# Kernel tuning notes

Hardware: AMD Instinct MI355X
Metric: run time of the kernel (lower is better)

## Reference

```python
import jax, jax.numpy as jnp
import numpy as np

B, T, D, S, K_FUT = 32, 1024, 1024, 256, 3


def setup_inputs() -> dict:
    key = jax.random.key(0)
    ks = jax.random.split(key, 8)
    sc = 1.0 / np.sqrt(D)
    return {
        "features": jax.random.normal(ks[0], (B, T, D), jnp.float32),
        "codebook": jax.random.uniform(ks[1], (S, D), jnp.float32, -1.0 / S, 1.0 / S),
        "W_ih": jax.random.normal(ks[2], (3 * D, D), jnp.float32) * sc,
        "W_hh": jax.random.normal(ks[3], (3 * D, D), jnp.float32) * sc,
        "b_ih": jnp.zeros((3 * D,), jnp.float32),
        "b_hh": jnp.zeros((3 * D,), jnp.float32),
        "W_p": jax.random.normal(ks[4], (D, D), jnp.float32) * sc,
        "b_p": jnp.zeros((D,), jnp.float32),
        "neg_idx": jax.random.randint(ks[5], (K_FUT, T, B), 0, B, jnp.int32),
    }


def _gru(x, W_ih, W_hh, b_ih, b_hh):
    # x: (B, T, D) -> outputs (B, T, D), torch nn.GRU gate math
    d = x.shape[-1]
    xs = jnp.swapaxes(x, 0, 1)  # (T, B, D)
    h0 = jnp.zeros((x.shape[0], d), x.dtype)

    def step(h, xt):
        gi = xt @ W_ih.T + b_ih
        gh = h @ W_hh.T + b_hh
        i_r, i_z, i_n = jnp.split(gi, 3, axis=-1)
        h_r, h_z, h_n = jnp.split(gh, 3, axis=-1)
        r = jax.nn.sigmoid(i_r + h_r)
        z = jax.nn.sigmoid(i_z + h_z)
        n = jnp.tanh(i_n + r * h_n)
        h_new = (1.0 - z) * n + z * h
        return h_new, h_new

    _, hs = jax.lax.scan(step, h0, xs)
    return jnp.swapaxes(hs, 0, 1)  # (B, T, D)


def _quantize(features, codebook):
    # argmin of euclidean distance == argmin of squared distance
    flat = features.reshape(-1, features.shape[-1])  # (B*T, D)
    d2 = (
        jnp.sum(flat * flat, -1, keepdims=True)
        - 2.0 * flat @ codebook.T
        + jnp.sum(codebook * codebook, -1)[None, :]
    )  # (B*T, S)
    idx = jnp.argmin(d2, axis=-1)
    quantized = codebook[idx].reshape(features.shape)
    return quantized, idx.reshape(features.shape[:2])


def _cp_loss(features, quantized, neg_idx, W_ih, W_hh, b_ih, b_hh, W_p, b_p):
    Bb, Tt, _ = features.shape
    H = _gru(quantized, W_ih, W_hh, b_ih, b_hh)
    Hp = H @ W_p.T + b_p  # (B, T, D)
    Zt = jnp.swapaxes(features, 0, 1)  # (T, B, D)
    K = min(K_FUT, Tt - 1)
    total = jnp.float32(0.0)
    for k in range(1, K + 1):
        pos = jnp.sum(Hp[:, : Tt - k] * features[:, k:], axis=-1)  # (B, T-k)
        idx = neg_idx[k - 1, : Tt - k]  # (T-k, B)
        negZ = jnp.take_along_axis(Zt[: Tt - k], idx[:, :, None], axis=1)  # (T-k, B, D)
        neg = jnp.sum(Hp[:, : Tt - k] * jnp.swapaxes(negZ, 0, 1), axis=-1)  # (B, T-k)
        per_tau = -jnp.log(jax.nn.sigmoid(pos - neg).mean(axis=0))  # (T-k,)
        total = total + per_tau.sum()
    return total / (K * (Tt - K))


def reference(features, codebook, W_ih, W_hh, b_ih, b_hh, W_p, b_p, neg_idx):
    quantized, indices = _quantize(features, codebook)
    cp = _cp_loss(features, quantized, neg_idx, W_ih, W_hh, b_ih, b_hh, W_p, b_p)
    sg = jax.lax.stop_gradient
    commitment = jnp.mean((sg(features) - quantized) ** 2)
    codebook_l = jnp.mean((features - sg(quantized)) ** 2)
    total = cp + commitment + 0.25 * codebook_l
    return quantized, indices, total
```

## Files before the change

kernel.cpp:

```cpp
#include <hip/hip_runtime.h>
#include <stdint.h>

#define DIM   1024
#define TLEN  1024
#define BATCH 32
#define NCODE 256

#define WS_CC   16
#define WS_IDX  272
#define WS_CGI  33040
#define WS_H    819472
#define WS_HP   34373904

#define OUT_IDX 33554432
#define OUT_TOT 33587200

__global__ __launch_bounds__(256) void k_norms(const float* __restrict__ cb,
                                               float* __restrict__ cc) {
  int c = blockIdx.x;
  int t = threadIdx.x;
  const float4* p = (const float4*)(cb + (size_t)c * DIM);
  float4 v = p[t];
  float s = v.x*v.x + v.y*v.y + v.z*v.z + v.w*v.w;
#pragma unroll
  for (int m = 1; m < 64; m <<= 1) s += __shfl_xor(s, m);
  __shared__ float ls[4];
  if ((t & 63) == 0) ls[t >> 6] = s;
  __syncthreads();
  if (t == 0) cc[c] = ls[0] + ls[1] + ls[2] + ls[3];
}

__global__ __launch_bounds__(256) void k_quant(
    const float* __restrict__ F, const float* __restrict__ CB,
    const float* __restrict__ cc, float* __restrict__ qout,
    float* __restrict__ idxf, int* __restrict__ idxi,
    float* __restrict__ sse_acc)
{
  __shared__ float Fl[32][33];
  __shared__ float Cl[256][33];
  __shared__ float ccl[256];
  __shared__ float sumff[32];
  __shared__ unsigned long long rowmin[32];
  __shared__ float wsum[4];

  const int tid = threadIdx.x;
  const size_t m0 = (size_t)blockIdx.x * 32;

  const int tm = tid >> 5;
  const int tn = tid & 31;
  const int ar = tid >> 3;
  const int ac = tid & 7;

  if (tid < 32) rowmin[tid] = ~0ull;
  ccl[tid] = cc[tid];

  float acc[4][8];
#pragma unroll
  for (int i = 0; i < 4; ++i)
#pragma unroll
    for (int j = 0; j < 8; ++j) acc[i][j] = 0.f;
  float ffp = 0.f;

  for (int k0 = 0; k0 < DIM; k0 += 32) {
    __syncthreads();
    {
      float4 v = *(const float4*)&F[(m0 + ar) * DIM + k0 + 4 * ac];
      Fl[ar][4*ac+0] = v.x; Fl[ar][4*ac+1] = v.y;
      Fl[ar][4*ac+2] = v.z; Fl[ar][4*ac+3] = v.w;
      ffp += v.x*v.x + v.y*v.y + v.z*v.z + v.w*v.w;
    }
#pragma unroll
    for (int rep = 0; rep < 8; ++rep) {
      int r = ar + 32 * rep;
      float4 v = *(const float4*)&CB[(size_t)r * DIM + k0 + 4 * ac];
      Cl[r][4*ac+0] = v.x; Cl[r][4*ac+1] = v.y;
      Cl[r][4*ac+2] = v.z; Cl[r][4*ac+3] = v.w;
    }
    __syncthreads();
    for (int kk = 0; kk < 32; ++kk) {
      float a[4], b[8];
#pragma unroll
      for (int i = 0; i < 4; ++i) a[i] = Fl[tm + 8*i][kk];
#pragma unroll
      for (int j = 0; j < 8; ++j) b[j] = Cl[tn + 32*j][kk];
#pragma unroll
      for (int i = 0; i < 4; ++i)
#pragma unroll
        for (int j = 0; j < 8; ++j) acc[i][j] += a[i] * b[j];
    }
  }
  {
    float s = ffp;
    s += __shfl_xor(s, 1); s += __shfl_xor(s, 2); s += __shfl_xor(s, 4);
    if (ac == 0) sumff[ar] = s;
  }
  __syncthreads();
#pragma unroll
  for (int i = 0; i < 4; ++i) {
    float sf = sumff[tm + 8*i];
    unsigned long long best = ~0ull;
#pragma unroll
    for (int j = 0; j < 8; ++j) {
      int c = tn + 32*j;
      float sc = (sf - 2.f * acc[i][j]) + ccl[c];
      unsigned ub = __float_as_uint(sc);
      ub = (ub & 0x80000000u) ? ~ub : (ub | 0x80000000u);
      unsigned long long key = ((unsigned long long)ub << 32) | (unsigned)c;
      if (key < best) best = key;
    }
    atomicMin(&rowmin[tm + 8*i], best);
  }
  __syncthreads();
  if (tid < 32) {
    int code = (int)(rowmin[tid] & 0xffffffffull);
    idxi[m0 + tid] = code;
    idxf[m0 + tid] = (float)code;
  }
  float ssep = 0.f;
  for (int r = 0; r < 32; ++r) {
    int code = (int)(rowmin[r] & 0xffffffffull);
    float4 q = *(const float4*)&CB[(size_t)code * DIM + 4 * tid];
    float4 f = *(const float4*)&F[(m0 + r) * DIM + 4 * tid];
    *(float4*)&qout[(m0 + r) * DIM + 4 * tid] = q;
    float dx = f.x-q.x, dy = f.y-q.y, dz = f.z-q.z, dw = f.w-q.w;
    ssep += dx*dx + dy*dy + dz*dz + dw*dw;
  }
  {
    float s = ssep;
#pragma unroll
    for (int m = 1; m < 64; m <<= 1) s += __shfl_xor(s, m);
    if ((tid & 63) == 0) wsum[tid >> 6] = s;
  }
  __syncthreads();
  if (tid == 0) atomicAdd(sse_acc, wsum[0] + wsum[1] + wsum[2] + wsum[3]);
}

template<int BM, int BN, int BK>
__global__ __launch_bounds__(256) void k_gemm_nt(
    const float* __restrict__ A, const float* __restrict__ B,
    const float* __restrict__ bias, float* __restrict__ C,
    int M, int N, int K)
{
  __shared__ float Al[BM][BK + 1];
  __shared__ float Bl[BN][BK + 1];
  const int tid = threadIdx.x;
  const int tm = tid >> 4;
  const int tn = tid & 15;
  const size_t m0 = (size_t)blockIdx.y * BM;
  const size_t n0 = (size_t)blockIdx.x * BN;
  float acc[BM/16][BN/16];
#pragma unroll
  for (int i = 0; i < BM/16; ++i)
#pragma unroll
    for (int j = 0; j < BN/16; ++j) acc[i][j] = 0.f;

  constexpr int F4R = BK / 4;
  for (int k0 = 0; k0 < K; k0 += BK) {
    __syncthreads();
    for (int rr = tid; rr < BM * F4R; rr += 256) {
      int r = rr / F4R, c4 = rr % F4R;
      float4 v = *(const float4*)&A[(m0 + r) * K + k0 + 4 * c4];
      Al[r][4*c4+0] = v.x; Al[r][4*c4+1] = v.y;
      Al[r][4*c4+2] = v.z; Al[r][4*c4+3] = v.w;
    }
    for (int rr = tid; rr < BN * F4R; rr += 256) {
      int r = rr / F4R, c4 = rr % F4R;
      float4 v = *(const float4*)&B[(n0 + r) * K + k0 + 4 * c4];
      Bl[r][4*c4+0] = v.x; Bl[r][4*c4+1] = v.y;
      Bl[r][4*c4+2] = v.z; Bl[r][4*c4+3] = v.w;
    }
    __syncthreads();
    for (int kk = 0; kk < BK; ++kk) {
      float a[BM/16], b[BN/16];
#pragma unroll
      for (int i = 0; i < BM/16; ++i) a[i] = Al[tm + 16*i][kk];
#pragma unroll
      for (int j = 0; j < BN/16; ++j) b[j] = Bl[tn + 16*j][kk];
#pragma unroll
      for (int i = 0; i < BM/16; ++i)
#pragma unroll
        for (int j = 0; j < BN/16; ++j) acc[i][j] += a[i] * b[j];
    }
  }
#pragma unroll
  for (int i = 0; i < BM/16; ++i)
#pragma unroll
    for (int j = 0; j < BN/16; ++j) {
      size_t cn = n0 + tn + 16*j;
      C[(m0 + tm + 16*i) * N + cn] = acc[i][j] + bias[cn];
    }
}

__global__ __launch_bounds__(1024, 4) void k_gru(
    const float* __restrict__ Whh, const float* __restrict__ bhh,
    const float* __restrict__ CGI, const int* __restrict__ idx,
    float* __restrict__ H, int* __restrict__ slots)
{
  __shared__ float ghl[16][3][8];

  const int tid = threadIdx.x;
  const int w   = tid >> 6;
  const int l   = tid & 63;
  const int m   = blockIdx.x & 63;
  const int g   = blockIdx.x >> 6;
  const int d   = (m << 4) + w;

  float wr[16], wz[16], wn[16];
  {
    const float* p0 = Whh + (size_t)d * DIM + (l << 4);
    const float* p1 = Whh + (size_t)(DIM + d) * DIM + (l << 4);
    const float* p2 = Whh + (size_t)(2 * DIM + d) * DIM + (l << 4);
#pragma unroll
    for (int q = 0; q < 4; ++q) {
      float4 a = ((const float4*)p0)[q];
      wr[4*q+0] = a.x; wr[4*q+1] = a.y; wr[4*q+2] = a.z; wr[4*q+3] = a.w;
      float4 b = ((const float4*)p1)[q];
      wz[4*q+0] = b.x; wz[4*q+1] = b.y; wz[4*q+2] = b.z; wz[4*q+3] = b.w;
      float4 c = ((const float4*)p2)[q];
      wn[4*q+0] = c.x; wn[4*q+1] = c.y; wn[4*q+2] = c.z; wn[4*q+3] = c.w;
    }
  }
  const float bhr = bhh[d];
  const float bhz = bhh[DIM + d];
  const float bhn = bhh[2 * DIM + d];

  const int eb = tid >> 4;
  const int ed = tid & 15;
  float hprev = 0.f;

  int* myslots = slots + (g << 6);

  for (int t = 0; t < TLEN; ++t) {
    float ir = 0.f, iz = 0.f, inn = 0.f;
    if (tid < 128) {
      int code = idx[(size_t)((g << 3) + eb) * TLEN + t];
      const float* cgi = CGI + (size_t)code * (3 * DIM) + (m << 4) + ed;
      ir  = cgi[0];
      iz  = cgi[DIM];
      inn = cgi[2 * DIM];
    }

    if (t > 0) {
      if (tid < 64) {
        long guard = 0;
        while (__hip_atomic_load(&myslots[tid], __ATOMIC_RELAXED,
                                 __HIP_MEMORY_SCOPE_AGENT) < t) {
          __builtin_amdgcn_s_sleep(2);
          if (++guard > 4000000L) break;
        }
        (void)__hip_atomic_load(&myslots[tid], __ATOMIC_ACQUIRE,
                                __HIP_MEMORY_SCOPE_AGENT);
      }
    }
    __syncthreads();

    if (t > 0) {
      float4 bufA[4], bufB[4];
#define LOADH(buf, bb)                                                        \
      {                                                                       \
        const float* hp = H + ((size_t)((g << 3) + (bb)) * TLEN + (t - 1))    \
                              * DIM + (l << 4);                               \
        buf[0] = ((const float4*)hp)[0];                                      \
        buf[1] = ((const float4*)hp)[1];                                      \
        buf[2] = ((const float4*)hp)[2];                                      \
        buf[3] = ((const float4*)hp)[3];                                      \
      }
#define DOTRED(buf, bb)                                                       \
      {                                                                       \
        float ar = 0.f, az = 0.f, an = 0.f;                                   \
        _Pragma("unroll")                                                     \
        for (int q = 0; q < 4; ++q) {                                         \
          const float4 h4 = buf[q];                                           \
          ar += h4.x*wr[4*q+0] + h4.y*wr[4*q+1] + h4.z*wr[4*q+2] + h4.w*wr[4*q+3]; \
          az += h4.x*wz[4*q+0] + h4.y*wz[4*q+1] + h4.z*wz[4*q+2] + h4.w*wz[4*q+3]; \
          an += h4.x*wn[4*q+0] + h4.y*wn[4*q+1] + h4.z*wn[4*q+2] + h4.w*wn[4*q+3]; \
        }                                                                     \
        _Pragma("unroll")                                                     \
        for (int s = 1; s < 64; s <<= 1) {                                    \
          ar += __shfl_xor(ar, s);                                            \
          az += __shfl_xor(az, s);                                            \
          an += __shfl_xor(an, s);                                            \
        }                                                                     \
        if (l == 0) {                                                         \
          ghl[w][0][bb] = ar + bhr;                                           \
          ghl[w][1][bb] = az + bhz;                                           \
          ghl[w][2][bb] = an + bhn;                                           \
        }                                                                     \
      }
      LOADH(bufA, 0)
      LOADH(bufB, 1)  DOTRED(bufA, 0)
      LOADH(bufA, 2)  DOTRED(bufB, 1)
      LOADH(bufB, 3)  DOTRED(bufA, 2)
      LOADH(bufA, 4)  DOTRED(bufB, 3)
      LOADH(bufB, 5)  DOTRED(bufA, 4)
      LOADH(bufA, 6)  DOTRED(bufB, 5)
      LOADH(bufB, 7)  DOTRED(bufA, 6)
                      DOTRED(bufB, 7)
#undef LOADH
#undef DOTRED
    } else {
      if (l == 0) {
#pragma unroll
        for (int b = 0; b < 8; ++b) {
          ghl[w][0][b] = bhr; ghl[w][1][b] = bhz; ghl[w][2][b] = bhn;
        }
      }
    }
    __syncthreads();

    if (tid < 128) {
      float gr = ghl[ed][0][eb];
      float gz = ghl[ed][1][eb];
      float gn = ghl[ed][2][eb];
      float r = 1.f / (1.f + expf(-(ir + gr)));
      float z = 1.f / (1.f + expf(-(iz + gz)));
      float n = tanhf(inn + r * gn);
      float hn = (1.f - z) * n + z * hprev;
      __hip_atomic_store(
          &H[((size_t)((g << 3) + eb) * TLEN + t) * DIM + (m << 4) + ed], hn,
          __ATOMIC_RELAXED, __HIP_MEMORY_SCOPE_AGENT);
      hprev = hn;
    }
    __syncthreads();
    if (tid == 0)
      __hip_atomic_store(&myslots[m], t + 1, __ATOMIC_RELEASE,
                         __HIP_MEMORY_SCOPE_AGENT);
  }
}

__global__ __launch_bounds__(256) void k_loss(
    const float* __restrict__ Hp, const float* __restrict__ F,
    const int* __restrict__ nidx, float* __restrict__ cp_acc)
{
  int blk = blockIdx.x;
  int k, t;
  if (blk < 1023)      { k = 1; t = blk; }
  else if (blk < 2045) { k = 2; t = blk - 1023; }
  else                 { k = 3; t = blk - 2045; }
  const int tid = threadIdx.x;
  const int wv = tid >> 6, l = tid & 63;
  __shared__ float ssum[4];
  float lsum = 0.f;
  for (int bi = 0; bi < 8; ++bi) {
    int b = wv * 8 + bi;
    const float4* hp = (const float4*)(Hp + (size_t)(b * TLEN + t) * DIM);
    const float4* fp = (const float4*)(F + (size_t)(b * TLEN + t + k) * DIM);
    int nb = nidx[(k - 1) * TLEN * BATCH + t * BATCH + b];
    const float4* fn = (const float4*)(F + (size_t)(nb * TLEN + t) * DIM);
    float pos = 0.f, neg = 0.f;
#pragma unroll
    for (int c = 0; c < 4; ++c) {
      float4 h4 = hp[l + 64 * c];
      float4 p4 = fp[l + 64 * c];
      float4 n4 = fn[l + 64 * c];
      pos += h4.x*p4.x + h4.y*p4.y + h4.z*p4.z + h4.w*p4.w;
      neg += h4.x*n4.x + h4.y*n4.y + h4.z*n4.z + h4.w*n4.w;
    }
#pragma unroll
    for (int m = 1; m < 64; m <<= 1) {
      pos += __shfl_xor(pos, m);
      neg += __shfl_xor(neg, m);
    }
    if (l == 0) lsum += 1.f / (1.f + expf(neg - pos));
  }
  if (l == 0) ssum[wv] = lsum;
  __syncthreads();
  if (tid == 0) {
    float mean = (ssum[0] + ssum[1] + ssum[2] + ssum[3]) * (1.f / 32.f);
    atomicAdd(cp_acc, -logf(mean));
  }
}

__global__ void k_final(const float* __restrict__ sse, const float* __restrict__ cp,
                        float* __restrict__ out) {
  out[0] = cp[0] * (1.f / 3063.f) + 1.25f * sse[0] * (1.f / 33554432.f);
}

extern "C" void kernel_launch(void* const* d_in, const int* in_sizes, int n_in,
                              void* d_out, int out_size, void* d_ws, size_t ws_size,
                              hipStream_t stream)
{
  const float* F    = (const float*)d_in[0];
  const float* CB   = (const float*)d_in[1];
  const float* Wih  = (const float*)d_in[2];
  const float* Whh  = (const float*)d_in[3];
  const float* bih  = (const float*)d_in[4];
  const float* bhh  = (const float*)d_in[5];
  const float* Wp   = (const float*)d_in[6];
  const float* bp   = (const float*)d_in[7];
  const int*   nidx = (const int*)d_in[8];
  float* out = (float*)d_out;
  float* ws  = (float*)d_ws;

  hipMemsetAsync(d_ws, 0, 64, stream);
  hipMemsetAsync((void*)((char*)d_ws + (size_t)WS_HP * 4), 0, 1024, stream);

  k_norms<<<NCODE, 256, 0, stream>>>(CB, ws + WS_CC);
  k_quant<<<1024, 256, 0, stream>>>(F, CB, ws + WS_CC, out,
                                    out + OUT_IDX, (int*)(ws + WS_IDX), ws + 1);
  k_gemm_nt<64,128,16><<<dim3(3072/128, 256/64), 256, 0, stream>>>(
      CB, Wih, bih, ws + WS_CGI, 256, 3072, 1024);
  k_gru<<<256, 1024, 0, stream>>>(Whh, bhh, ws + WS_CGI,
                                  (const int*)(ws + WS_IDX), ws + WS_H,
                                  (int*)(ws + WS_HP));
  k_gemm_nt<64,128,16><<<dim3(1024/128, 32768/64), 256, 0, stream>>>(
      ws + WS_H, Wp, bp, ws + WS_HP, 32768, 1024, 1024);
  k_loss<<<3066, 256, 0, stream>>>(ws + WS_HP, F, nidx, ws + 2);
  k_final<<<1, 1, 0, stream>>>(ws + 1, ws + 2, out + OUT_TOT);
}
```

Baseline: 15.17 ms.

## Split GRU recurrence sync into per-batch-pair flags and prefetch input gates

The GRU step is split into four phases, each covering two batch rows. Each phase waits only on that pair's readiness flags from all blocks in the group, so dependent work can start before a full timestep finishes everywhere. The token indices are staged in LDS up front, and the next step's input-gate values are prefetched right after publishing h. This adds more __syncthreads per step, a larger flag array and a much shorter spin-guard timeout, which could break out early and read stale data under contention.

```diff
diff --git a/kernel.cpp b/kernel.cpp
--- a/kernel.cpp
+++ b/kernel.cpp
@@ -197,6 +197,7 @@
     float* __restrict__ H, int* __restrict__ slots)
 {
   __shared__ float ghl[16][3][8];
+  __shared__ int   idxl[8][TLEN];
 
   const int tid = threadIdx.x;
   const int w   = tid >> 6;
@@ -224,107 +225,113 @@
   const float bhz = bhh[DIM + d];
   const float bhn = bhh[2 * DIM + d];
 
-  const int eb = tid >> 4;
-  const int ed = tid & 15;
+  for (int i = tid; i < 8 * TLEN; i += 1024)
+    idxl[i >> 10][i & 1023] = idx[(size_t)((g << 3) + (i >> 10)) * TLEN + (i & 1023)];
+
+  const int bq = l >> 4;
+  const int ed = l & 15;
+  const int myb = 2 * w + bq;
+  const bool epi = (w < 4) && (l < 32);
   float hprev = 0.f;
 
-  int* myslots = slots + (g << 6);
+  int* gslots = slots + ((size_t)g << 11);
+
+  __syncthreads();
+
+  float pir = 0.f, piz = 0.f, pin = 0.f;
+  if (epi) {
+    int code = idxl[myb][0];
+    const float* cgi = CGI + (size_t)code * (3 * DIM) + (m << 4) + ed;
+    pir = cgi[0]; piz = cgi[DIM]; pin = cgi[2 * DIM];
+  }
 
   for (int t = 0; t < TLEN; ++t) {
-    float ir = 0.f, iz = 0.f, inn = 0.f;
-    if (tid < 128) {
-      int code = idx[(size_t)((g << 3) + eb) * TLEN + t];
-      const float* cgi = CGI + (size_t)code * (3 * DIM) + (m << 4) + ed;
-      ir  = cgi[0];
-      iz  = cgi[DIM];
-      inn = cgi[2 * DIM];
-    }
-
-    if (t > 0) {
-      if (tid < 64) {
+#pragma unroll
+    for (int q = 0; q < 4; ++q) {
+      if (t > 0 && w == q) {
         long guard = 0;
-        while (__hip_atomic_load(&myslots[tid], __ATOMIC_RELAXED,
+        while (__hip_atomic_load(&gslots[(l << 5) + q], __ATOMIC_RELAXED,
                                  __HIP_MEMORY_SCOPE_AGENT) < t) {
-          __builtin_amdgcn_s_sleep(2);
-          if (++guard > 4000000L) break;
-        }
-        (void)__hip_atomic_load(&myslots[tid], __ATOMIC_ACQUIRE,
+          __builtin_amdgcn_s_sleep(4);
+          if (++guard > 20000L) break;
+        }
+        (void)__hip_atomic_load(&gslots[(l << 5) + q], __ATOMIC_ACQUIRE,
                                 __HIP_MEMORY_SCOPE_AGENT);
       }
-    }
-    __syncthreads();
-
-    if (t > 0) {
-      float4 bufA[4], bufB[4];
+      __syncthreads();
+
+      if (t > 0) {
+        float4 bufA[4], bufB[4];
 #define LOADH(buf, bb)                                                        \
-      {                                                                       \
-        const float* hp = H + ((size_t)((g << 3) + (bb)) * TLEN + (t - 1))    \
-                              * DIM + (l << 4);                               \
-        buf[0] = ((const float4*)hp)[0];                                      \
-        buf[1] = ((const float4*)hp)[1];                                      \
-        buf[2] = ((const float4*)hp)[2];                                      \
-        buf[3] = ((const float4*)hp)[3];                                      \
-      }
+        {                                                                     \
+          const float* hp = H + ((size_t)((g << 3) + (bb)) * TLEN + (t - 1))  \
+                                * DIM + (l << 4);                             \
+          buf[0] = ((const float4*)hp)[0];                                    \
+          buf[1] = ((const float4*)hp)[1];                                    \
+          buf[2] = ((const float4*)hp)[2];                                    \
+          buf[3] = ((const float4*)hp)[3];                                    \
+        }
 #define DOTRED(buf, bb)                                                       \
-      {                                                                       \
-        float ar = 0.f, az = 0.f, an = 0.f;                                   \
-        _Pragma("unroll")                                                     \
-        for (int q = 0; q < 4; ++q) {                                         \
-          const float4 h4 = buf[q];                                           \
-          ar += h4.x*wr[4*q+0] + h4.y*wr[4*q+1] + h4.z*wr[4*q+2] + h4.w*wr[4*q+3]; \
-          az += h4.x*wz[4*q+0] + h4.y*wz[4*q+1] + h4.z*wz[4*q+2] + h4.w*wz[4*q+3]; \
-          an += h4.x*wn[4*q+0] + h4.y*wn[4*q+1] + h4.z*wn[4*q+2] + h4.w*wn[4*q+3]; \
-        }                                                                     \
-        _Pragma("unroll")                                                     \
-        for (int s = 1; s < 64; s <<= 1) {                                    \
-          ar += __shfl_xor(ar, s);                                            \
-          az += __shfl_xor(az, s);                                            \
-          an += __shfl_xor(an, s);                                            \
-        }                                                                     \
-        if (l == 0) {                                                         \
-          ghl[w][0][bb] = ar + bhr;                                           \
-          ghl[w][1][bb] = az + bhz;                                           \
-          ghl[w][2][bb] = an + bhn;                                           \
-        }                                                                     \
-      }
-      LOADH(bufA, 0)
-      LOADH(bufB, 1)  DOTRED(bufA, 0)
-      LOADH(bufA, 2)  DOTRED(bufB, 1)
-      LOADH(bufB, 3)  DOTRED(bufA, 2)
-      LOADH(bufA, 4)  DOTRED(bufB, 3)
-      LOADH(bufB, 5)  DOTRED(bufA, 4)
-      LOADH(bufA, 6)  DOTRED(bufB, 5)
-      LOADH(bufB, 7)  DOTRED(bufA, 6)
-                      DOTRED(bufB, 7)
+        {                                                                     \
+          float ar = 0.f, az = 0.f, an = 0.f;                                 \
+          _Pragma("unroll")                                                   \
+          for (int qq = 0; qq < 4; ++qq) {                                    \
+            const float4 h4 = buf[qq];                                        \
+            ar += h4.x*wr[4*qq+0] + h4.y*wr[4*qq+1] + h4.z*wr[4*qq+2] + h4.w*wr[4*qq+3]; \
+            az += h4.x*wz[4*qq+0] + h4.y*wz[4*qq+1] + h4.z*wz[4*qq+2] + h4.w*wz[4*qq+3]; \
+            an += h4.x*wn[4*qq+0] + h4.y*wn[4*qq+1] + h4.z*wn[4*qq+2] + h4.w*wn[4*qq+3]; \
+          }                                                                   \
+          _Pragma("unroll")                                                   \
+          for (int s = 1; s < 64; s <<= 1) {                                  \
+            ar += __shfl_xor(ar, s);                                          \
+            az += __shfl_xor(az, s);                                          \
+            an += __shfl_xor(an, s);                                          \
+          }                                                                   \
+          if (l == 0) {                                                       \
+            ghl[w][0][bb] = ar + bhr;                                         \
+            ghl[w][1][bb] = az + bhz;                                         \
+            ghl[w][2][bb] = an + bhn;                                         \
+          }                                                                   \
+        }
+        LOADH(bufA, 2 * q)
+        LOADH(bufB, 2 * q + 1)
+        DOTRED(bufA, 2 * q)
+        DOTRED(bufB, 2 * q + 1)
 #undef LOADH
 #undef DOTRED
-    } else {
-      if (l == 0) {
-#pragma unroll
-        for (int b = 0; b < 8; ++b) {
-          ghl[w][0][b] = bhr; ghl[w][1][b] = bhz; ghl[w][2][b] = bhn;
+      } else {
+        if (l == 0) {
+          ghl[w][0][2*q]   = bhr; ghl[w][1][2*q]   = bhz; ghl[w][2][2*q]   = bhn;
+          ghl[w][0][2*q+1] = bhr; ghl[w][1][2*q+1] = bhz; ghl[w][2][2*q+1] = bhn;
         }
       }
-    }
-    __syncthreads();
-
-    if (tid < 128) {
-      float gr = ghl[ed][0][eb];
-      float gz = ghl[ed][1][eb];
-      float gn = ghl[ed][2][eb];
-      float r = 1.f / (1.f + expf(-(ir + gr)));
-      float z = 1.f / (1.f + expf(-(iz + gz)));
-      float n = tanhf(inn + r * gn);
-      float hn = (1.f - z) * n + z * hprev;
-      __hip_atomic_store(
-          &H[((size_t)((g << 3) + eb) * TLEN + t) * DIM + (m << 4) + ed], hn,
-          __ATOMIC_RELAXED, __HIP_MEMORY_SCOPE_AGENT);
-      hprev = hn;
-    }
-    __syncthreads();
-    if (tid == 0)
-      __hip_atomic_store(&myslots[m], t + 1, __ATOMIC_RELEASE,
-                         __HIP_MEMORY_SCOPE_AGENT);
+      __syncthreads();
+
+      if (w == q) {
+        if (l < 32) {
+          float gr = ghl[ed][0][myb];
+          float gz = ghl[ed][1][myb];
+          float gn = ghl[ed][2][myb];
+          float r = 1.f / (1.f + expf(-(pir + gr)));
+          float z = 1.f / (1.f + expf(-(piz + gz)));
+          float n = tanhf(pin + r * gn);
+          float hn = (1.f - z) * n + z * hprev;
+          __hip_atomic_store(
+              &H[((size_t)((g << 3) + myb) * TLEN + t) * DIM + (m << 4) + ed],
+              hn, __ATOMIC_RELAXED, __HIP_MEMORY_SCOPE_AGENT);
+          hprev = hn;
+        }
+        if (l == 0)
+          __hip_atomic_store(&gslots[(m << 5) + q], t + 1, __ATOMIC_RELEASE,
+                             __HIP_MEMORY_SCOPE_AGENT);
+        __builtin_amdgcn_sched_barrier(0);
+        if (l < 32 && t + 1 < TLEN) {
+          int code = idxl[myb][t + 1];
+          const float* cgi = CGI + (size_t)code * (3 * DIM) + (m << 4) + ed;
+          pir = cgi[0]; piz = cgi[DIM]; pin = cgi[2 * DIM];
+        }
+      }
+    }
   }
 }
 
@@ -393,7 +400,7 @@
   float* ws  = (float*)d_ws;
 
   hipMemsetAsync(d_ws, 0, 64, stream);
-  hipMemsetAsync((void*)((char*)d_ws + (size_t)WS_HP * 4), 0, 1024, stream);
+  hipMemsetAsync((void*)((char*)d_ws + (size_t)WS_HP * 4), 0, 32768, stream);
 
   k_norms<<<NCODE, 256, 0, stream>>>(CB, ws + WS_CC);
   k_quant<<<1024, 256, 0, stream>>>(F, CB, ws + WS_CC, out,
```

Result: slower. 25.58 ms (+68.6%).

## Tighten GRU cross-block sync with padded flags, relaxed atomics and prefetched inputs

Applied to the files above, without the earlier changes.

Reworks the persistent GRU step loop. Sequence indices are staged in shared memory, and the next step's input-gate values are prefetched after each store. The gate update is done by one wave handling two elements each, with 64-bit packed stores. The per-block completion flag is written right after a vmcnt wait instead of after an extra block barrier, and flags are padded to separate 128-byte lines with a larger memset. H is read through relaxed 64-bit atomic loads without the acquire load. This shortens the per-timestep critical path of the serial recurrence, at the cost of weaker memory ordering that relies on the waitcnt for visibility.

```diff
diff --git a/kernel.cpp b/kernel.cpp
--- a/kernel.cpp
+++ b/kernel.cpp
@@ -197,6 +197,7 @@
     float* __restrict__ H, int* __restrict__ slots)
 {
   __shared__ float ghl[16][3][8];
+  __shared__ int   idxl[8][TLEN];
 
   const int tid = threadIdx.x;
   const int w   = tid >> 6;
@@ -224,56 +225,58 @@
   const float bhz = bhh[DIM + d];
   const float bhn = bhh[2 * DIM + d];
 
-  const int eb = tid >> 4;
-  const int ed = tid & 15;
-  float hprev = 0.f;
-
-  int* myslots = slots + (g << 6);
+  for (int i = tid; i < 8 * TLEN; i += 1024)
+    idxl[i >> 10][i & 1023] = idx[(size_t)((g << 3) + (i >> 10)) * TLEN + (i & 1023)];
+
+  const int eb = l >> 3;
+  const int e2 = l & 7;
+  float hprev0 = 0.f, hprev1 = 0.f;
+
+  int* gslots = slots + ((size_t)g << 11);
+
+  __syncthreads();
+
+  float2 pir2 = {0.f,0.f}, piz2 = {0.f,0.f}, pin2 = {0.f,0.f};
+  if (tid < 64) {
+    int code = idxl[eb][0];
+    const float2* cgi2 = (const float2*)(CGI + (size_t)code * (3 * DIM) + (m << 4));
+    pir2 = cgi2[e2];
+    piz2 = cgi2[512 + e2];
+    pin2 = cgi2[1024 + e2];
+  }
 
   for (int t = 0; t < TLEN; ++t) {
-    float ir = 0.f, iz = 0.f, inn = 0.f;
-    if (tid < 128) {
-      int code = idx[(size_t)((g << 3) + eb) * TLEN + t];
-      const float* cgi = CGI + (size_t)code * (3 * DIM) + (m << 4) + ed;
-      ir  = cgi[0];
-      iz  = cgi[DIM];
-      inn = cgi[2 * DIM];
-    }
+    if (t > 0 && tid < 64) {
+      long guard = 0;
+      while (__hip_atomic_load(&gslots[l << 5], __ATOMIC_RELAXED,
+                               __HIP_MEMORY_SCOPE_AGENT) < t) {
+        __builtin_amdgcn_s_sleep(1);
+        if (++guard > 2000000L) break;
+      }
+    }
+    __syncthreads();
 
     if (t > 0) {
-      if (tid < 64) {
-        long guard = 0;
-        while (__hip_atomic_load(&myslots[tid], __ATOMIC_RELAXED,
-                                 __HIP_MEMORY_SCOPE_AGENT) < t) {
-          __builtin_amdgcn_s_sleep(2);
-          if (++guard > 4000000L) break;
-        }
-        (void)__hip_atomic_load(&myslots[tid], __ATOMIC_ACQUIRE,
-                                __HIP_MEMORY_SCOPE_AGENT);
-      }
-    }
-    __syncthreads();
-
-    if (t > 0) {
-      float4 bufA[4], bufB[4];
+      unsigned long long bufA[8], bufB[8];
 #define LOADH(buf, bb)                                                        \
       {                                                                       \
-        const float* hp = H + ((size_t)((g << 3) + (bb)) * TLEN + (t - 1))    \
-                              * DIM + (l << 4);                               \
-        buf[0] = ((const float4*)hp)[0];                                      \
-        buf[1] = ((const float4*)hp)[1];                                      \
-        buf[2] = ((const float4*)hp)[2];                                      \
-        buf[3] = ((const float4*)hp)[3];                                      \
+        const unsigned long long* hp = (const unsigned long long*)            \
+            (H + ((size_t)((g << 3) + (bb)) * TLEN + (t - 1)) * DIM + (l << 4)); \
+        _Pragma("unroll")                                                     \
+        for (int q8 = 0; q8 < 8; ++q8)                                        \
+          buf[q8] = __hip_atomic_load(hp + q8, __ATOMIC_RELAXED,              \
+                                      __HIP_MEMORY_SCOPE_AGENT);              \
       }
 #define DOTRED(buf, bb)                                                       \
       {                                                                       \
         float ar = 0.f, az = 0.f, an = 0.f;                                   \
         _Pragma("unroll")                                                     \
-        for (int q = 0; q < 4; ++q) {                                         \
-          const float4 h4 = buf[q];                                           \
-          ar += h4.x*wr[4*q+0] + h4.y*wr[4*q+1] + h4.z*wr[4*q+2] + h4.w*wr[4*q+3]; \
-          az += h4.x*wz[4*q+0] + h4.y*wz[4*q+1] + h4.z*wz[4*q+2] + h4.w*wz[4*q+3]; \
-          an += h4.x*wn[4*q+0] + h4.y*wn[4*q+1] + h4.z*wn[4*q+2] + h4.w*wn[4*q+3]; \
+        for (int q8 = 0; q8 < 8; ++q8) {                                      \
+          float h0 = __uint_as_float((unsigned)buf[q8]);                      \
+          float h1 = __uint_as_float((unsigned)(buf[q8] >> 32));              \
+          ar += h0 * wr[2*q8] + h1 * wr[2*q8+1];                              \
+          az += h0 * wz[2*q8] + h1 * wz[2*q8+1];                              \
+          an += h0 * wn[2*q8] + h1 * wn[2*q8+1];                              \
         }                                                                     \
         _Pragma("unroll")                                                     \
         for (int s = 1; s < 64; s <<= 1) {                                    \
@@ -308,23 +311,36 @@
     }
     __syncthreads();
 
-    if (tid < 128) {
-      float gr = ghl[ed][0][eb];
-      float gz = ghl[ed][1][eb];
-      float gn = ghl[ed][2][eb];
-      float r = 1.f / (1.f + expf(-(ir + gr)));
-      float z = 1.f / (1.f + expf(-(iz + gz)));
-      float n = tanhf(inn + r * gn);
-      float hn = (1.f - z) * n + z * hprev;
+    if (tid < 64) {
+      float gr0 = ghl[2*e2+0][0][eb], gz0 = ghl[2*e2+0][1][eb], gn0 = ghl[2*e2+0][2][eb];
+      float gr1 = ghl[2*e2+1][0][eb], gz1 = ghl[2*e2+1][1][eb], gn1 = ghl[2*e2+1][2][eb];
+      float r0 = 1.f / (1.f + expf(-(pir2.x + gr0)));
+      float z0 = 1.f / (1.f + expf(-(piz2.x + gz0)));
+      float n0 = tanhf(pin2.x + r0 * gn0);
+      float hn0 = (1.f - z0) * n0 + z0 * hprev0;
+      float r1 = 1.f / (1.f + expf(-(pir2.y + gr1)));
+      float z1 = 1.f / (1.f + expf(-(piz2.y + gz1)));
+      float n1 = tanhf(pin2.y + r1 * gn1);
+      float hn1 = (1.f - z1) * n1 + z1 * hprev1;
+      hprev0 = hn0; hprev1 = hn1;
+      unsigned long long hv =
+          ((unsigned long long)__float_as_uint(hn1) << 32) | __float_as_uint(hn0);
       __hip_atomic_store(
-          &H[((size_t)((g << 3) + eb) * TLEN + t) * DIM + (m << 4) + ed], hn,
-          __ATOMIC_RELAXED, __HIP_MEMORY_SCOPE_AGENT);
-      hprev = hn;
-    }
-    __syncthreads();
-    if (tid == 0)
-      __hip_atomic_store(&myslots[m], t + 1, __ATOMIC_RELEASE,
-                         __HIP_MEMORY_SCOPE_AGENT);
+          (unsigned long long*)&H[((size_t)((g << 3) + eb) * TLEN + t) * DIM
+                                  + (m << 4) + 2 * e2],
+          hv, __ATOMIC_RELAXED, __HIP_MEMORY_SCOPE_AGENT);
+      asm volatile("s_waitcnt vmcnt(0)" ::: "memory");
+      if (l == 0)
+        __hip_atomic_store(&gslots[m << 5], t + 1, __ATOMIC_RELAXED,
+                           __HIP_MEMORY_SCOPE_AGENT);
+      if (t + 1 < TLEN) {
+        int code = idxl[eb][t + 1];
+        const float2* cgi2 = (const float2*)(CGI + (size_t)code * (3 * DIM) + (m << 4));
+        pir2 = cgi2[e2];
+        piz2 = cgi2[512 + e2];
+        pin2 = cgi2[1024 + e2];
+      }
+    }
   }
 }
 
@@ -393,7 +409,7 @@
   float* ws  = (float*)d_ws;
 
   hipMemsetAsync(d_ws, 0, 64, stream);
-  hipMemsetAsync((void*)((char*)d_ws + (size_t)WS_HP * 4), 0, 1024, stream);
+  hipMemsetAsync((void*)((char*)d_ws + (size_t)WS_HP * 4), 0, 32768, stream);
 
   k_norms<<<NCODE, 256, 0, stream>>>(CB, ws + WS_CC);
   k_quant<<<1024, 256, 0, stream>>>(F, CB, ws + WS_CC, out,
```

After: 39.77 ms. +162.1%, slower.
